# Kernel tuning notes

Hardware: AMD Instinct MI355X
Metric: run time of the kernel (lower is better)

The kernel has to match this reference:

```python
import jax, jax.numpy as jnp
import numpy as np

E = 262144   # num edges
T = 1048576  # num triplets
H = 128      # hidden_channels
IE = 64      # int_emb_size
NR = 6       # num_radial
NS = 7       # num_spherical
BD = 8       # basis_emb_size_dist
BA = 8       # basis_emb_size_angle


def setup_inputs() -> dict:
    key = jax.random.key(0)
    ks = jax.random.split(key, 32)
    def rnd(k, shape, s=0.1):
        return jax.random.normal(k, shape, dtype=jnp.float32) * s
    return {
        "x1": rnd(ks[0], (T, H), 1.0),
        "x_old": rnd(ks[1], (E, H), 1.0),
        "rbf0": rnd(ks[2], (E, NR), 1.0),
        "sbf": rnd(ks[3], (T, NS * NR), 1.0),
        "idx_kj": jax.random.randint(ks[4], (T,), 0, E),
        "idx_ji": jax.random.randint(ks[5], (T,), 0, E),
        "W_rbf1": rnd(ks[6], (NR, BD)),
        "W_rbf2": rnd(ks[7], (BD, H)),
        "W_sbf1": rnd(ks[8], (NS * NR, BA)),
        "W_sbf2": rnd(ks[9], (BA, IE)),
        "W_rbf": rnd(ks[10], (NR, H)),
        "W_kj": rnd(ks[11], (H, H)), "b_kj": rnd(ks[12], (H,)),
        "W_ji": rnd(ks[13], (H, H)), "b_ji": rnd(ks[14], (H,)),
        "W_connect": rnd(ks[15], (H, H)), "b_connect": rnd(ks[16], (H,)),
        "W_get_up": rnd(ks[17], (H, H)), "b_get_up": rnd(ks[18], (H,)),
        "W_down": rnd(ks[19], (H, IE)), "b_down": rnd(ks[20], (IE,)),
        "W_up": rnd(ks[21], (IE, H)), "b_up": rnd(ks[22], (H,)),
        "res_before_W": rnd(ks[23], (1, 2, H, H)), "res_before_b": rnd(ks[24], (1, 2, H)),
        "W_lin": rnd(ks[25], (H, H)), "b_lin": rnd(ks[26], (H,)),
        "res_after_W": rnd(ks[27], (2, 2, H, H)), "res_after_b": rnd(ks[28], (2, 2, H)),
    }


def _residual(x, W, b):
    # x + act(lin2(act(lin1(x))))
    h = jax.nn.silu(x @ W[0] + b[0])
    return x + jax.nn.silu(h @ W[1] + b[1])


def reference(x1, x_old, rbf0, sbf, idx_kj, idx_ji, W_rbf1, W_rbf2, W_sbf1, W_sbf2,
              W_rbf, W_kj, b_kj, W_ji, b_ji, W_connect, b_connect, W_get_up, b_get_up,
              W_down, b_down, W_up, b_up, res_before_W, res_before_b, W_lin, b_lin,
              res_after_W, res_after_b):
    act = jax.nn.silu  # swish
    nE = x_old.shape[0]
    # aggregate plane features onto edges
    x_up = jax.ops.segment_sum(x1, idx_ji, num_segments=nE)
    x_up = act(x_up @ W_get_up + b_get_up)
    x_ji = act(x_old @ W_ji + b_ji)
    x_kj = act(x_old @ W_kj + b_kj)
    rbf = (rbf0 @ W_rbf1) @ W_rbf2            # [E, H]
    x_kj = x_kj * rbf
    x_kj = act(x_kj @ W_down + b_down)        # [E, IE]
    sbf_p = (sbf @ W_sbf1) @ W_sbf2           # [T, IE]
    x_kj = x_kj[idx_kj] * sbf_p               # gather edges -> triplets
    x_kj = jax.ops.segment_sum(x_kj, idx_ji, num_segments=nE)  # scatter back to edges
    x_kj = act(x_kj @ W_up + b_up)
    e1 = x_ji + x_kj
    e1 = act(e1 @ W_connect + b_connect) + x_up
    for i in range(res_before_W.shape[0]):
        e1 = _residual(e1, res_before_W[i], res_before_b[i])
    e1 = act(e1 @ W_lin + b_lin) + x_old
    for i in range(res_after_W.shape[0]):
        e1 = _residual(e1, res_after_W[i], res_after_b[i])
    e2 = (rbf0 @ W_rbf) * e1
    return (e1, e2)
```

## Files before the change

### kernel.cpp

```cpp
#include <hip/hip_runtime.h>

#define E_N 262144
#define T_N 1048576

typedef short  bf16x8  __attribute__((ext_vector_type(8)));
typedef float  f32x4   __attribute__((ext_vector_type(4)));

#define OFF_KJ    0
#define OFF_DOWN  16384
#define OFF_UP    24576
#define OFF_JI    32768
#define OFF_GU    49152
#define OFF_CN    65536
#define OFF_RB0   81920
#define OFF_RB1   98304
#define OFF_LIN   114688
#define OFF_RA00  131072
#define OFF_RA01  147456
#define OFF_RA10  163840
#define OFF_RA11  180224
#define OFF_END   196608
#define WREG_BYTES 524288u

#define OFFB_AGG   0u
#define OFFB_XKJ   33554432u
#define OFFB_WREG  67108864u
#define OFFB_CNT   67633152u
#define OFFB_POS   68683776u
#define OFFB_TRI   69732352u
#define OFFB_BS    73926656u
#define OFFB_BP    73927680u
#define OFFB_KJP   75497472u
#define OFFB_INV   79691776u

__device__ __forceinline__ float silu_f(float x) {
  float e;
  asm("v_exp_f32_e32 %0, %1" : "=v"(e) : "v"(x * -1.44269504088896f));
  float r;
  asm("v_rcp_f32_e32 %0, %1" : "=v"(r) : "v"(1.0f + e));
  return x * r;
}

__device__ __forceinline__ unsigned short f2bf(float f) {
  union { float f; unsigned int u; } v; v.f = f;
  unsigned int u = v.u;
  return (unsigned short)((u + 0x7fffu + ((u >> 16) & 1u)) >> 16);
}
__device__ __forceinline__ float bf2f(unsigned short h) {
  union { unsigned int u; float f; } v; v.u = ((unsigned int)h) << 16;
  return v.f;
}

__device__ __forceinline__ unsigned cvtpk(float lo, float hi) {
  unsigned r;
  asm("v_cvt_pk_bf16_f32 %0, %1, %2" : "=v"(r) : "v"(lo), "v"(hi));
  return r;
}

template<int NC, int NR, int NTH>
__device__ __forceinline__ void stage_tile(const float* __restrict__ g, char* __restrict__ lds) {
  constexpr int RB = NC * 2;
  constexpr int C4 = NC / 4;
  for (int i = threadIdx.x; i < NR * C4; i += NTH) {
    int r = i / C4, c4 = i % C4;
    float4 v = *(const float4*)(g + (size_t)r * NC + c4 * 4);
    uint2 u;
    u.x = cvtpk(v.x, v.y);
    u.y = cvtpk(v.z, v.w);
    *(uint2*)(lds + r * RB + ((c4 * 8) ^ ((r & 7) << 4))) = u;
  }
}

template<int MREP, int NREP, int KSTEPS, int RB>
__device__ __forceinline__ void mfma_gemm(const char* __restrict__ lds, int row0, int col0,
                                          const unsigned short* __restrict__ WT, int lane,
                                          f32x4 (&acc)[MREP][NREP]) {
  const int kg = lane >> 4, r15 = lane & 15;
#pragma unroll
  for (int m = 0; m < MREP; ++m)
#pragma unroll
    for (int n = 0; n < NREP; ++n) acc[m][n] = (f32x4){0.f, 0.f, 0.f, 0.f};
  __builtin_amdgcn_s_setprio(1);
#pragma unroll
  for (int kk = 0; kk < KSTEPS; ++kk) {
    bf16x8 a[MREP], bfr[NREP];
#pragma unroll
    for (int m = 0; m < MREP; ++m) {
      int row = row0 + m * 16 + r15;
      a[m] = *(const bf16x8*)(lds + row * RB + ((kk * 64 + kg * 16) ^ ((row & 7) << 4)));
    }
#pragma unroll
    for (int n = 0; n < NREP; ++n) {
      int nc = col0 + n * 16 + r15;
      bfr[n] = *(const bf16x8*)((const short*)WT + nc * (KSTEPS * 32) + kk * 32 + kg * 8);
    }
#pragma unroll
    for (int m = 0; m < MREP; ++m)
#pragma unroll
      for (int n = 0; n < NREP; ++n)
        acc[m][n] = __builtin_amdgcn_mfma_f32_16x16x32_bf16(a[m], bfr[n], acc[m][n], 0, 0, 0);
  }
  __builtin_amdgcn_s_setprio(0);
}

template<int MREP, int NREP, int KSTEPS, int RS>
__device__ __forceinline__ void mfma_gemm_gA(const unsigned short* __restrict__ gA,
                                             int row0, int col0,
                                             const unsigned short* __restrict__ WT, int lane,
                                             f32x4 (&acc)[MREP][NREP]) {
  const int kg = lane >> 4, r15 = lane & 15;
#pragma unroll
  for (int m = 0; m < MREP; ++m)
#pragma unroll
    for (int n = 0; n < NREP; ++n) acc[m][n] = (f32x4){0.f, 0.f, 0.f, 0.f};
  __builtin_amdgcn_s_setprio(1);
#pragma unroll
  for (int kk = 0; kk < KSTEPS; ++kk) {
    bf16x8 a[MREP], bfr[NREP];
#pragma unroll
    for (int m = 0; m < MREP; ++m)
      a[m] = *(const bf16x8*)(gA + (size_t)(row0 + m * 16 + r15) * RS + kk * 32 + kg * 8);
#pragma unroll
    for (int n = 0; n < NREP; ++n) {
      int nc = col0 + n * 16 + r15;
      bfr[n] = *(const bf16x8*)((const short*)WT + nc * (KSTEPS * 32) + kk * 32 + kg * 8);
    }
#pragma unroll
    for (int m = 0; m < MREP; ++m)
#pragma unroll
      for (int n = 0; n < NREP; ++n)
        acc[m][n] = __builtin_amdgcn_mfma_f32_16x16x32_bf16(a[m], bfr[n], acc[m][n], 0, 0, 0);
  }
  __builtin_amdgcn_s_setprio(0);
}

template<int RB>
__device__ __forceinline__ void write_cd(char* __restrict__ lds, int wrow, int wcol, int lane,
                                         const f32x4 (&v)[2][2]) {
  const int kg = lane >> 4, r15 = lane & 15;
#pragma unroll
  for (int m = 0; m < 2; ++m)
#pragma unroll
    for (int n = 0; n < 2; ++n) {
      int col2 = (wcol + n * 16 + r15) * 2;
      int row0 = wrow + m * 16 + kg * 4;
      unsigned u0 = cvtpk(v[m][n][0], v[m][n][1]);
      unsigned u1 = cvtpk(v[m][n][2], v[m][n][3]);
      *(unsigned short*)(lds + (row0 + 0) * RB + (col2 ^ (((row0 + 0) & 7) << 4))) = (unsigned short)u0;
      *(unsigned short*)(lds + (row0 + 1) * RB + (col2 ^ (((row0 + 1) & 7) << 4))) = (unsigned short)(u0 >> 16);
      *(unsigned short*)(lds + (row0 + 2) * RB + (col2 ^ (((row0 + 2) & 7) << 4))) = (unsigned short)u1;
      *(unsigned short*)(lds + (row0 + 3) * RB + (col2 ^ (((row0 + 3) & 7) << 4))) = (unsigned short)(u1 >> 16);
    }
}

__global__ void __launch_bounds__(256) k_prep(
    const float* __restrict__ W_kj, const float* __restrict__ W_down,
    const float* __restrict__ W_up, const float* __restrict__ W_ji,
    const float* __restrict__ W_get_up, const float* __restrict__ W_connect,
    const float* __restrict__ rbW, const float* __restrict__ W_lin,
    const float* __restrict__ raW,
    const float* __restrict__ W_rbf1, const float* __restrict__ W_rbf2,
    unsigned short* __restrict__ wreg) {
  int b = blockIdx.x;
  if (b == 13) {
    float* W12 = (float*)(wreg + OFF_END);
    for (int i = threadIdx.x; i < 768; i += 256) {
      int r = i >> 7, n = i & 127;
      float s = 0.f;
#pragma unroll
      for (int q = 0; q < 8; ++q) s += W_rbf1[r * 8 + q] * W_rbf2[q * 128 + n];
      W12[i] = s;
    }
    return;
  }
  const float* src; int K = 128, N = 128; int off;
  switch (b) {
    case 0:  src = W_kj;          off = OFF_KJ;  break;
    case 1:  src = W_down;        off = OFF_DOWN; N = 64;  break;
    case 2:  src = W_up;          off = OFF_UP;   K = 64;  break;
    case 3:  src = W_ji;          off = OFF_JI;  break;
    case 4:  src = W_get_up;      off = OFF_GU;  break;
    case 5:  src = W_connect;     off = OFF_CN;  break;
    case 6:  src = rbW;           off = OFF_RB0; break;
    case 7:  src = rbW + 16384;   off = OFF_RB1; break;
    case 8:  src = W_lin;         off = OFF_LIN; break;
    case 9:  src = raW;           off = OFF_RA00; break;
    case 10: src = raW + 16384;   off = OFF_RA01; break;
    case 11: src = raW + 32768;   off = OFF_RA10; break;
    default: src = raW + 49152;   off = OFF_RA11; break;
  }
  unsigned short* dst = wreg + off;
  for (int i = threadIdx.x; i < K * N; i += 256) {
    int k = i / N, n = i % N;
    dst[n * K + k] = f2bf(src[i]);
  }
}

__global__ void __launch_bounds__(256) k_hist(const int* __restrict__ idx_ji,
                                              int* __restrict__ counts) {
  int t = blockIdx.x * 256 + threadIdx.x;
  atomicAdd(&counts[idx_ji[t]], 1);
}

__global__ void __launch_bounds__(1024) k_scan1(const int* __restrict__ counts,
                                                int* __restrict__ locpre,
                                                int* __restrict__ bsum) {
  __shared__ int s[1024];
  int i = blockIdx.x * 1024 + threadIdx.x;
  int v = counts[i];
  s[threadIdx.x] = v; __syncthreads();
  for (int o = 1; o < 1024; o <<= 1) {
    int t = (threadIdx.x >= o) ? s[threadIdx.x - o] : 0;
    __syncthreads();
    s[threadIdx.x] += t;
    __syncthreads();
  }
  locpre[i] = s[threadIdx.x] - v;
  if (threadIdx.x == 1023) bsum[blockIdx.x] = s[1023];
}

__global__ void __launch_bounds__(256) k_scan2(const int* __restrict__ bsum,
                                               int* __restrict__ bpre, int* __restrict__ offs) {
  __shared__ int s[256];
  int v = bsum[threadIdx.x];
  s[threadIdx.x] = v; __syncthreads();
  for (int o = 1; o < 256; o <<= 1) {
    int t = (threadIdx.x >= o) ? s[threadIdx.x - o] : 0;
    __syncthreads();
    s[threadIdx.x] += t;
    __syncthreads();
  }
  bpre[threadIdx.x] = s[threadIdx.x] - v;
  if (threadIdx.x == 0) offs[E_N] = T_N;
}

__global__ void __launch_bounds__(1024) k_scan3(const int* __restrict__ locpre,
                                                const int* __restrict__ bpre,
                                                int* __restrict__ offs,
                                                int* __restrict__ pos) {
  int i = blockIdx.x * 1024 + threadIdx.x;
  int v = locpre[i] + bpre[blockIdx.x];
  offs[i] = v;
  pos[i] = v;
}

__global__ void __launch_bounds__(256) k_fill(const int* __restrict__ idx_ji,
                                              const int* __restrict__ idx_kj,
                                              int* __restrict__ pos,
                                              int* __restrict__ tri,
                                              int* __restrict__ inv,
                                              int* __restrict__ kjp) {
  int t = blockIdx.x * 256 + threadIdx.x;
  int e = idx_ji[t];
  int slot = atomicAdd(&pos[e], 1);
  tri[slot] = t;
  inv[t] = slot;
  kjp[slot] = idx_kj[t];
}

__global__ void __launch_bounds__(256) k_sbfp(const float* __restrict__ sbf,
                                              const float* __restrict__ W_sbf1,
                                              const float* __restrict__ W_sbf2,
                                              const int* __restrict__ inv,
                                              unsigned int* __restrict__ sbfp) {
  __shared__ float s_s[336];
  __shared__ float s_t8[8][8];
  int t0 = blockIdx.x * 8;
  const float4* src = (const float4*)(sbf + (size_t)t0 * 42);
  for (int i = threadIdx.x; i < 84; i += 256)
    ((float4*)s_s)[i] = src[i];
  __syncthreads();
  if (threadIdx.x < 64) {
    int w8 = threadIdx.x >> 3, bb = threadIdx.x & 7;
    float s = 0.f;
#pragma unroll
    for (int r = 0; r < 42; ++r) s += s_s[w8 * 42 + r] * W_sbf1[r * 8 + bb];
    s_t8[w8][bb] = s;
  }
  __syncthreads();
  int w8 = threadIdx.x >> 5, jj = threadIdx.x & 31;
  float sp0 = 0.f, sp1 = 0.f;
#pragma unroll
  for (int bb = 0; bb < 8; ++bb) {
    float tv = s_t8[w8][bb];
    sp0 += tv * W_sbf2[bb * 64 + jj * 2];
    sp1 += tv * W_sbf2[bb * 64 + jj * 2 + 1];
  }
  int slot = inv[t0 + w8];
  sbfp[(size_t)slot * 32 + jj] = cvtpk(sp0, sp1);
}

__global__ void __launch_bounds__(256) k_aggB(const int* __restrict__ offs,
                                              const int* __restrict__ kjp,
                                              const unsigned int* __restrict__ sbfp,
                                              const unsigned int* __restrict__ xkj,
                                              unsigned int* __restrict__ agg) {
  int sub = threadIdx.x >> 5, jj = threadIdx.x & 31;
  int e = blockIdx.x * 8 + sub;
  int o0 = offs[e], o1 = offs[e + 1];
  float a0 = 0.f, a1 = 0.f;
  for (int i = o0; i < o1; ++i) {
    int kj = kjp[i];
    unsigned int sv = sbfp[(size_t)i * 32 + jj];
    unsigned int xv = xkj[(size_t)kj * 32 + jj];
    a0 += bf2f((unsigned short)(sv & 0xffff)) * bf2f((unsigned short)(xv & 0xffff));
    a1 += bf2f((unsigned short)(sv >> 16)) * bf2f((unsigned short)(xv >> 16));
  }
  agg[(size_t)e * 32 + jj] = cvtpk(a0, a1);
}

__global__ void __launch_bounds__(256) k_xupg(const int* __restrict__ offs,
                                              const int* __restrict__ tri,
                                              const float* __restrict__ x1,
                                              unsigned int* __restrict__ out) {
  int sub = threadIdx.x >> 6, h2 = threadIdx.x & 63;
  int e = blockIdx.x * 4 + sub;
  int o0 = offs[e], o1 = offs[e + 1];
  float a0 = 0.f, a1 = 0.f;
  for (int i = o0; i < o1; ++i) {
    int t = tri[i];
    float2 v = *(const float2*)(x1 + (size_t)t * 128 + h2 * 2);
    a0 += v.x; a1 += v.y;
  }
  out[(size_t)e * 128 + h2] = cvtpk(a0, a1);
}

__global__ void __launch_bounds__(512, 4) phaseA(
    const float* __restrict__ x_old, const float* __restrict__ rbf0,
    const unsigned short* __restrict__ wreg,
    const float* __restrict__ b_kj, const float* __restrict__ b_down,
    unsigned short* __restrict__ xkjdown) {
  __shared__ char lds[32768];
  char* B0 = lds;
  char* B1 = lds + 16384;
  const int tid = threadIdx.x, lane = tid & 63, wave = tid >> 6;
  const int kg = lane >> 4, r15 = lane & 15;
  const int wrow = (wave >> 2) * 32, wcol = (wave & 3) * 32;
  const size_t e_base = (size_t)blockIdx.x * 64;
  const float* W12 = (const float*)(wreg + OFF_END);

  stage_tile<128, 64, 512>(x_old + e_base * 128, B0);
  __syncthreads();

  f32x4 acc[2][2], val[2][2];
  mfma_gemm<2, 2, 4, 256>(B0, wrow, wcol, wreg + OFF_KJ, lane, acc);
#pragma unroll
  for (int n = 0; n < 2; ++n) {
    int col = wcol + n * 16 + r15;
    float bk = b_kj[col];
    float wc[6];
#pragma unroll
    for (int q = 0; q < 6; ++q) wc[q] = W12[q * 128 + col];
#pragma unroll
    for (int m = 0; m < 2; ++m)
#pragma unroll
      for (int r = 0; r < 4; ++r) {
        int row = wrow + m * 16 + kg * 4 + r;
        const float* rp = rbf0 + (e_base + row) * 6;
        float rv = rp[0]*wc[0] + rp[1]*wc[1] + rp[2]*wc[2] + rp[3]*wc[3] + rp[4]*wc[4] + rp[5]*wc[5];
        val[m][n][r] = silu_f(acc[m][n][r] + bk) * rv;
      }
  }
  write_cd<256>(B1, wrow, wcol, lane, val);
  __syncthreads();

  const int wrow2 = (wave >> 1) * 16, wcol2 = (wave & 1) * 32;
  f32x4 a2[1][2];
  mfma_gemm<1, 2, 4, 256>(B1, wrow2, wcol2, wreg + OFF_DOWN, lane, a2);
#pragma unroll
  for (int n = 0; n < 2; ++n) {
    int col = wcol2 + n * 16 + r15;
    float bd = b_down[col];
#pragma unroll
    for (int r = 0; r < 4; ++r) {
      int row = wrow2 + kg * 4 + r;
      xkjdown[(e_base + row) * 64 + col] = f2bf(silu_f(a2[0][n][r] + bd));
    }
  }
}

__global__ void __launch_bounds__(512, 4) phaseC1(
    const float* __restrict__ x_old, float* __restrict__ e1buf,
    const unsigned short* __restrict__ xup_b,
    const unsigned short* __restrict__ agg, const unsigned short* __restrict__ wreg,
    const float* __restrict__ b_up, const float* __restrict__ b_ji,
    const float* __restrict__ b_get_up, const float* __restrict__ b_connect,
    const float* __restrict__ rbB, const float* __restrict__ b_lin,
    const float* __restrict__ raB,
    const float* __restrict__ rbf0, const float* __restrict__ W_rbf,
    float* __restrict__ e2o) {
  __shared__ char lds[32768];
  char* X0 = lds;
  char* X1 = lds + 16384;
  const int tid = threadIdx.x, lane = tid & 63, wave = tid >> 6;
  const int kg = lane >> 4, r15 = lane & 15;
  const int wrow = (wave >> 2) * 32, wcol = (wave & 3) * 32;
  const size_t e_base = (size_t)blockIdx.x * 64;

  stage_tile<128, 64, 512>(x_old + e_base * 128, X1);
  __syncthreads();

  f32x4 acc[2][2], keep[2][2], h[2][2];

  mfma_gemm_gA<2, 2, 2, 64>(agg + e_base * 64, wrow, wcol, wreg + OFF_UP, lane, acc);
#pragma unroll
  for (int n = 0; n < 2; ++n) {
    float bu = b_up[wcol + n * 16 + r15];
#pragma unroll
    for (int m = 0; m < 2; ++m)
#pragma unroll
      for (int r = 0; r < 4; ++r) h[m][n][r] = silu_f(acc[m][n][r] + bu);
  }
  mfma_gemm<2, 2, 4, 256>(X1, wrow, wcol, wreg + OFF_JI, lane, acc);
#pragma unroll
  for (int n = 0; n < 2; ++n) {
    float bj = b_ji[wcol + n * 16 + r15];
#pragma unroll
    for (int m = 0; m < 2; ++m)
#pragma unroll
      for (int r = 0; r < 4; ++r) keep[m][n][r] = silu_f(acc[m][n][r] + bj) + h[m][n][r];
  }
  write_cd<256>(X0, wrow, wcol, lane, keep);
  __syncthreads();

  mfma_gemm_gA<2, 2, 4, 256>(xup_b + e_base * 256, wrow, wcol, wreg + OFF_GU, lane, acc);
#pragma unroll
  for (int n = 0; n < 2; ++n) {
    float bg = b_get_up[wcol + n * 16 + r15];
#pragma unroll
    for (int m = 0; m < 2; ++m)
#pragma unroll
      for (int r = 0; r < 4; ++r) h[m][n][r] = silu_f(acc[m][n][r] + bg);
  }
  mfma_gemm<2, 2, 4, 256>(X0, wrow, wcol, wreg + OFF_CN, lane, acc);
#pragma unroll
  for (int n = 0; n < 2; ++n) {
    float bc = b_connect[wcol + n * 16 + r15];
#pragma unroll
    for (int m = 0; m < 2; ++m)
#pragma unroll
      for (int r = 0; r < 4; ++r) keep[m][n][r] = silu_f(acc[m][n][r] + bc) + h[m][n][r];
  }
  write_cd<256>(X1, wrow, wcol, lane, keep);
  __syncthreads();

  mfma_gemm<2, 2, 4, 256>(X1, wrow, wcol, wreg + OFF_RB0, lane, acc);
#pragma unroll
  for (int n = 0; n < 2; ++n) {
    float bv = rbB[wcol + n * 16 + r15];
#pragma unroll
    for (int m = 0; m < 2; ++m)
#pragma unroll
      for (int r = 0; r < 4; ++r) h[m][n][r] = silu_f(acc[m][n][r] + bv);
  }
  write_cd<256>(X0, wrow, wcol, lane, h);
  __syncthreads();

  mfma_gemm<2, 2, 4, 256>(X0, wrow, wcol, wreg + OFF_RB1, lane, acc);
#pragma unroll
  for (int n = 0; n < 2; ++n) {
    float bv = rbB[128 + wcol + n * 16 + r15];
#pragma unroll
    for (int m = 0; m < 2; ++m)
#pragma unroll
      for (int r = 0; r < 4; ++r) keep[m][n][r] += silu_f(acc[m][n][r] + bv);
  }
  write_cd<256>(X1, wrow, wcol, lane, keep);
  __syncthreads();

  mfma_gemm<2, 2, 4, 256>(X1, wrow, wcol, wreg + OFF_LIN, lane, acc);
#pragma unroll
  for (int n = 0; n < 2; ++n) {
    int col = wcol + n * 16 + r15;
    float bl = b_lin[col];
#pragma unroll
    for (int m = 0; m < 2; ++m)
#pragma unroll
      for (int r = 0; r < 4; ++r) {
        int row = wrow + m * 16 + kg * 4 + r;
        keep[m][n][r] = silu_f(acc[m][n][r] + bl) + x_old[(e_base + row) * 128 + col];
      }
  }
  write_cd<256>(X0, wrow, wcol, lane, keep);
  __syncthreads();

  mfma_gemm<2, 2, 4, 256>(X0, wrow, wcol, wreg + OFF_RA00, lane, acc);
#pragma unroll
  for (int n = 0; n < 2; ++n) {
    float bv = raB[wcol + n * 16 + r15];
#pragma unroll
    for (int m = 0; m < 2; ++m)
#pragma unroll
      for (int r = 0; r < 4; ++r) h[m][n][r] = silu_f(acc[m][n][r] + bv);
  }
  write_cd<256>(X1, wrow, wcol, lane, h);
  __syncthreads();

  mfma_gemm<2, 2, 4, 256>(X1, wrow, wcol, wreg + OFF_RA01, lane, acc);
#pragma unroll
  for (int n = 0; n < 2; ++n) {
    float bv = raB[128 + wcol + n * 16 + r15];
#pragma unroll
    for (int m = 0; m < 2; ++m)
#pragma unroll
      for (int r = 0; r < 4; ++r) keep[m][n][r] += silu_f(acc[m][n][r] + bv);
  }
  write_cd<256>(X0, wrow, wcol, lane, keep);
  __syncthreads();

  mfma_gemm<2, 2, 4, 256>(X0, wrow, wcol, wreg + OFF_RA10, lane, acc);
#pragma unroll
  for (int n = 0; n < 2; ++n) {
    float bv = raB[256 + wcol + n * 16 + r15];
#pragma unroll
    for (int m = 0; m < 2; ++m)
#pragma unroll
      for (int r = 0; r < 4; ++r) h[m][n][r] = silu_f(acc[m][n][r] + bv);
  }
  write_cd<256>(X1, wrow, wcol, lane, h);
  __syncthreads();

  mfma_gemm<2, 2, 4, 256>(X1, wrow, wcol, wreg + OFF_RA11, lane, acc);
#pragma unroll
  for (int n = 0; n < 2; ++n) {
    int col = wcol + n * 16 + r15;
    float bv = raB[384 + col];
    float wc[6];
#pragma unroll
    for (int q = 0; q < 6; ++q) wc[q] = W_rbf[q * 128 + col];
#pragma unroll
    for (int m = 0; m < 2; ++m)
#pragma unroll
      for (int r = 0; r < 4; ++r) {
        int row = wrow + m * 16 + kg * 4 + r;
        size_t e = e_base + row;
        float val = keep[m][n][r] + silu_f(acc[m][n][r] + bv);
        e1buf[e * 128 + col] = val;
        if (e2o) {
          const float* rp = rbf0 + e * 6;
          float rv = rp[0]*wc[0] + rp[1]*wc[1] + rp[2]*wc[2] + rp[3]*wc[3] + rp[4]*wc[4] + rp[5]*wc[5];
          e2o[e * 128 + col] = val * rv;
        }
      }
  }
}

__global__ void __launch_bounds__(256) k_e2(const float* __restrict__ e1,
                                            const float* __restrict__ rbf0,
                                            const float* __restrict__ W_rbf,
                                            float* __restrict__ e2) {
  size_t gid = (size_t)blockIdx.x * 256 + threadIdx.x;
  int e = (int)(gid >> 5);
  int c = (int)(gid & 31) << 2;
  float r6[6];
#pragma unroll
  for (int r = 0; r < 6; ++r) r6[r] = rbf0[(size_t)e * 6 + r];
  float4 v = *(const float4*)(e1 + (size_t)e * 128 + c);
  float4 o;
  float rv;
  rv = 0.f;
#pragma unroll
  for (int r = 0; r < 6; ++r) rv += r6[r] * W_rbf[r * 128 + c + 0];
  o.x = v.x * rv;
  rv = 0.f;
#pragma unroll
  for (int r = 0; r < 6; ++r) rv += r6[r] * W_rbf[r * 128 + c + 1];
  o.y = v.y * rv;
  rv = 0.f;
#pragma unroll
  for (int r = 0; r < 6; ++r) rv += r6[r] * W_rbf[r * 128 + c + 2];
  o.z = v.z * rv;
  rv = 0.f;
#pragma unroll
  for (int r = 0; r < 6; ++r) rv += r6[r] * W_rbf[r * 128 + c + 3];
  o.w = v.w * rv;
  *(float4*)(e2 + (size_t)e * 128 + c) = o;
}

extern "C" void kernel_launch(void* const* d_in, const int* in_sizes, int n_in,
                              void* d_out, int out_size, void* d_ws, size_t ws_size,
                              hipStream_t stream) {
  const float* x1        = (const float*)d_in[0];
  const float* x_old     = (const float*)d_in[1];
  const float* rbf0      = (const float*)d_in[2];
  const float* sbf       = (const float*)d_in[3];
  const int*   idx_kj    = (const int*)d_in[4];
  const int*   idx_ji    = (const int*)d_in[5];
  const float* W_rbf1    = (const float*)d_in[6];
  const float* W_rbf2    = (const float*)d_in[7];
  const float* W_sbf1    = (const float*)d_in[8];
  const float* W_sbf2    = (const float*)d_in[9];
  const float* W_rbf     = (const float*)d_in[10];
  const float* W_kj      = (const float*)d_in[11];
  const float* b_kj      = (const float*)d_in[12];
  const float* W_ji      = (const float*)d_in[13];
  const float* b_ji      = (const float*)d_in[14];
  const float* W_connect = (const float*)d_in[15];
  const float* b_connect = (const float*)d_in[16];
  const float* W_get_up  = (const float*)d_in[17];
  const float* b_get_up  = (const float*)d_in[18];
  const float* W_down    = (const float*)d_in[19];
  const float* b_down    = (const float*)d_in[20];
  const float* W_up      = (const float*)d_in[21];
  const float* b_up      = (const float*)d_in[22];
  const float* rbW       = (const float*)d_in[23];
  const float* rbB       = (const float*)d_in[24];
  const float* W_lin     = (const float*)d_in[25];
  const float* b_lin     = (const float*)d_in[26];
  const float* raW       = (const float*)d_in[27];
  const float* raB       = (const float*)d_in[28];

  float* e1buf = (float*)d_out;
  char*  base2 = (char*)d_out + (size_t)E_N * 128 * 4;
  float* e2out = (float*)base2;

  unsigned short* xkj_b = (unsigned short*)(base2 + OFFB_XKJ);
  int* counts = (int*)(base2 + OFFB_CNT);
  int* pos    = (int*)(base2 + OFFB_POS);
  int* tri    = (int*)(base2 + OFFB_TRI);
  int* bsum   = (int*)(base2 + OFFB_BS);
  int* bpre   = (int*)(base2 + OFFB_BP);
  int* kjp    = (int*)(base2 + OFFB_KJP);
  int* inv    = (int*)(base2 + OFFB_INV);

  const size_t need_ws = (size_t)WREG_BYTES + (size_t)E_N * 64 * 2;
  const bool fuse = ws_size >= need_ws;
  unsigned short* wreg  = fuse ? (unsigned short*)d_ws
                               : (unsigned short*)(base2 + OFFB_WREG);
  unsigned short* agg_b = fuse ? (unsigned short*)((char*)d_ws + WREG_BYTES)
                               : (unsigned short*)(base2 + OFFB_AGG);

  unsigned int* sbfp_u = (unsigned int*)e1buf;
  unsigned int* xup_u  = (unsigned int*)e1buf;

  k_prep<<<14, 256, 0, stream>>>(W_kj, W_down, W_up, W_ji, W_get_up, W_connect,
                                 rbW, W_lin, raW, W_rbf1, W_rbf2, wreg);

  hipMemsetAsync(counts, 0, (E_N + 1) * sizeof(int), stream);
  k_hist<<<T_N / 256, 256, 0, stream>>>(idx_ji, counts);
  k_scan1<<<256, 1024, 0, stream>>>(counts, pos, bsum);
  k_scan2<<<1, 256, 0, stream>>>(bsum, bpre, counts);
  k_scan3<<<256, 1024, 0, stream>>>(pos, bpre, counts, pos);
  k_fill<<<T_N / 256, 256, 0, stream>>>(idx_ji, idx_kj, pos, tri, inv, kjp);

  k_sbfp<<<T_N / 8, 256, 0, stream>>>(sbf, W_sbf1, W_sbf2, inv, sbfp_u);

  phaseA<<<E_N / 64, 512, 0, stream>>>(x_old, rbf0, wreg, b_kj, b_down, xkj_b);

  k_aggB<<<E_N / 8, 256, 0, stream>>>(counts, kjp, sbfp_u,
                                      (const unsigned int*)xkj_b, (unsigned int*)agg_b);

  k_xupg<<<E_N / 4, 256, 0, stream>>>(counts, tri, x1, xup_u);

  phaseC1<<<E_N / 64, 512, 0, stream>>>(x_old, e1buf, (const unsigned short*)xup_u,
                                        agg_b, wreg,
                                        b_up, b_ji, b_get_up, b_connect, rbB, b_lin, raB,
                                        rbf0, W_rbf, fuse ? e2out : nullptr);
  if (!fuse)
    k_e2<<<E_N * 32 / 256, 256, 0, stream>>>(e1buf, rbf0, W_rbf, e2out);
}
```

Before: 1.279 ms.

## Retile phaseC1 to 128-edge blocks of 1024 threads with 64x16 wave tiles

The fused edge MLP chain kernel now handles 128 edges per block with 16 waves instead of 64 edges with 8 waves. Each wave computes a 64x16 output tile (four M repeats, one N repeat) instead of 32x32, and the LDS ping-pong buffers double to 64KB. The goal is fewer blocks and more B-fragment reuse across M per weight load, at the cost of larger LDS per block, fewer resident blocks per CU, and more A-operand loads from LDS per wave.

```diff
diff --git a/kernel.cpp b/kernel.cpp
--- a/kernel.cpp
+++ b/kernel.cpp
@@ -134,14 +134,14 @@
   __builtin_amdgcn_s_setprio(0);
 }
 
-template<int RB>
+template<int MREP, int NREP, int RB>
 __device__ __forceinline__ void write_cd(char* __restrict__ lds, int wrow, int wcol, int lane,
-                                         const f32x4 (&v)[2][2]) {
+                                         const f32x4 (&v)[MREP][NREP]) {
   const int kg = lane >> 4, r15 = lane & 15;
 #pragma unroll
-  for (int m = 0; m < 2; ++m)
-#pragma unroll
-    for (int n = 0; n < 2; ++n) {
+  for (int m = 0; m < MREP; ++m)
+#pragma unroll
+    for (int n = 0; n < NREP; ++n) {
       int col2 = (wcol + n * 16 + r15) * 2;
       int row0 = wrow + m * 16 + kg * 4;
       unsigned u0 = cvtpk(v[m][n][0], v[m][n][1]);
@@ -361,7 +361,7 @@
         val[m][n][r] = silu_f(acc[m][n][r] + bk) * rv;
       }
   }
-  write_cd<256>(B1, wrow, wcol, lane, val);
+  write_cd<2, 2, 256>(B1, wrow, wcol, lane, val);
   __syncthreads();
 
   const int wrow2 = (wave >> 1) * 16, wcol2 = (wave & 1) * 32;
@@ -379,7 +379,7 @@
   }
 }
 
-__global__ void __launch_bounds__(512, 4) phaseC1(
+__global__ void __launch_bounds__(1024, 4) phaseC1(
     const float* __restrict__ x_old, float* __restrict__ e1buf,
     const unsigned short* __restrict__ xup_b,
     const unsigned short* __restrict__ agg, const unsigned short* __restrict__ wreg,
@@ -389,152 +389,141 @@
     const float* __restrict__ raB,
     const float* __restrict__ rbf0, const float* __restrict__ W_rbf,
     float* __restrict__ e2o) {
-  __shared__ char lds[32768];
+  __shared__ char lds[65536];
   char* X0 = lds;
-  char* X1 = lds + 16384;
+  char* X1 = lds + 32768;
   const int tid = threadIdx.x, lane = tid & 63, wave = tid >> 6;
   const int kg = lane >> 4, r15 = lane & 15;
-  const int wrow = (wave >> 2) * 32, wcol = (wave & 3) * 32;
-  const size_t e_base = (size_t)blockIdx.x * 64;
-
-  stage_tile<128, 64, 512>(x_old + e_base * 128, X1);
-  __syncthreads();
-
-  f32x4 acc[2][2], keep[2][2], h[2][2];
-
-  mfma_gemm_gA<2, 2, 2, 64>(agg + e_base * 64, wrow, wcol, wreg + OFF_UP, lane, acc);
-#pragma unroll
-  for (int n = 0; n < 2; ++n) {
-    float bu = b_up[wcol + n * 16 + r15];
-#pragma unroll
-    for (int m = 0; m < 2; ++m)
-#pragma unroll
-      for (int r = 0; r < 4; ++r) h[m][n][r] = silu_f(acc[m][n][r] + bu);
-  }
-  mfma_gemm<2, 2, 4, 256>(X1, wrow, wcol, wreg + OFF_JI, lane, acc);
-#pragma unroll
-  for (int n = 0; n < 2; ++n) {
-    float bj = b_ji[wcol + n * 16 + r15];
-#pragma unroll
-    for (int m = 0; m < 2; ++m)
-#pragma unroll
-      for (int r = 0; r < 4; ++r) keep[m][n][r] = silu_f(acc[m][n][r] + bj) + h[m][n][r];
-  }
-  write_cd<256>(X0, wrow, wcol, lane, keep);
-  __syncthreads();
-
-  mfma_gemm_gA<2, 2, 4, 256>(xup_b + e_base * 256, wrow, wcol, wreg + OFF_GU, lane, acc);
-#pragma unroll
-  for (int n = 0; n < 2; ++n) {
-    float bg = b_get_up[wcol + n * 16 + r15];
-#pragma unroll
-    for (int m = 0; m < 2; ++m)
-#pragma unroll
-      for (int r = 0; r < 4; ++r) h[m][n][r] = silu_f(acc[m][n][r] + bg);
-  }
-  mfma_gemm<2, 2, 4, 256>(X0, wrow, wcol, wreg + OFF_CN, lane, acc);
-#pragma unroll
-  for (int n = 0; n < 2; ++n) {
-    float bc = b_connect[wcol + n * 16 + r15];
-#pragma unroll
-    for (int m = 0; m < 2; ++m)
-#pragma unroll
-      for (int r = 0; r < 4; ++r) keep[m][n][r] = silu_f(acc[m][n][r] + bc) + h[m][n][r];
-  }
-  write_cd<256>(X1, wrow, wcol, lane, keep);
-  __syncthreads();
-
-  mfma_gemm<2, 2, 4, 256>(X1, wrow, wcol, wreg + OFF_RB0, lane, acc);
-#pragma unroll
-  for (int n = 0; n < 2; ++n) {
-    float bv = rbB[wcol + n * 16 + r15];
-#pragma unroll
-    for (int m = 0; m < 2; ++m)
-#pragma unroll
-      for (int r = 0; r < 4; ++r) h[m][n][r] = silu_f(acc[m][n][r] + bv);
-  }
-  write_cd<256>(X0, wrow, wcol, lane, h);
-  __syncthreads();
-
-  mfma_gemm<2, 2, 4, 256>(X0, wrow, wcol, wreg + OFF_RB1, lane, acc);
-#pragma unroll
-  for (int n = 0; n < 2; ++n) {
-    float bv = rbB[128 + wcol + n * 16 + r15];
-#pragma unroll
-    for (int m = 0; m < 2; ++m)
-#pragma unroll
-      for (int r = 0; r < 4; ++r) keep[m][n][r] += silu_f(acc[m][n][r] + bv);
-  }
-  write_cd<256>(X1, wrow, wcol, lane, keep);
-  __syncthreads();
-
-  mfma_gemm<2, 2, 4, 256>(X1, wrow, wcol, wreg + OFF_LIN, lane, acc);
-#pragma unroll
-  for (int n = 0; n < 2; ++n) {
-    int col = wcol + n * 16 + r15;
+  const int wrow = (wave >> 3) * 64;
+  const int wcol = (wave & 7) * 16;
+  const size_t e_base = (size_t)blockIdx.x * 128;
+
+  stage_tile<128, 128, 1024>(x_old + e_base * 128, X1);
+  __syncthreads();
+
+  f32x4 acc[4][1], keep[4][1], h[4][1];
+
+  mfma_gemm_gA<4, 1, 2, 64>(agg + e_base * 64, wrow, wcol, wreg + OFF_UP, lane, acc);
+#pragma unroll
+  for (int m = 0; m < 4; ++m) {
+    float bu = b_up[wcol + r15];
+#pragma unroll
+    for (int r = 0; r < 4; ++r) h[m][0][r] = silu_f(acc[m][0][r] + bu);
+  }
+  mfma_gemm<4, 1, 4, 256>(X1, wrow, wcol, wreg + OFF_JI, lane, acc);
+  {
+    float bj = b_ji[wcol + r15];
+#pragma unroll
+    for (int m = 0; m < 4; ++m)
+#pragma unroll
+      for (int r = 0; r < 4; ++r) keep[m][0][r] = silu_f(acc[m][0][r] + bj) + h[m][0][r];
+  }
+  write_cd<4, 1, 256>(X0, wrow, wcol, lane, keep);
+  __syncthreads();
+
+  mfma_gemm_gA<4, 1, 4, 256>(xup_b + e_base * 256, wrow, wcol, wreg + OFF_GU, lane, acc);
+  {
+    float bg = b_get_up[wcol + r15];
+#pragma unroll
+    for (int m = 0; m < 4; ++m)
+#pragma unroll
+      for (int r = 0; r < 4; ++r) h[m][0][r] = silu_f(acc[m][0][r] + bg);
+  }
+  mfma_gemm<4, 1, 4, 256>(X0, wrow, wcol, wreg + OFF_CN, lane, acc);
+  {
+    float bc = b_connect[wcol + r15];
+#pragma unroll
+    for (int m = 0; m < 4; ++m)
+#pragma unroll
+      for (int r = 0; r < 4; ++r) keep[m][0][r] = silu_f(acc[m][0][r] + bc) + h[m][0][r];
+  }
+  write_cd<4, 1, 256>(X1, wrow, wcol, lane, keep);
+  __syncthreads();
+
+  mfma_gemm<4, 1, 4, 256>(X1, wrow, wcol, wreg + OFF_RB0, lane, acc);
+  {
+    float bv = rbB[wcol + r15];
+#pragma unroll
+    for (int m = 0; m < 4; ++m)
+#pragma unroll
+      for (int r = 0; r < 4; ++r) h[m][0][r] = silu_f(acc[m][0][r] + bv);
+  }
+  write_cd<4, 1, 256>(X0, wrow, wcol, lane, h);
+  __syncthreads();
+
+  mfma_gemm<4, 1, 4, 256>(X0, wrow, wcol, wreg + OFF_RB1, lane, acc);
+  {
+    float bv = rbB[128 + wcol + r15];
+#pragma unroll
+    for (int m = 0; m < 4; ++m)
+#pragma unroll
+      for (int r = 0; r < 4; ++r) keep[m][0][r] += silu_f(acc[m][0][r] + bv);
+  }
+  write_cd<4, 1, 256>(X1, wrow, wcol, lane, keep);
+  __syncthreads();
+
+  mfma_gemm<4, 1, 4, 256>(X1, wrow, wcol, wreg + OFF_LIN, lane, acc);
+  {
+    int col = wcol + r15;
     float bl = b_lin[col];
 #pragma unroll
-    for (int m = 0; m < 2; ++m)
+    for (int m = 0; m < 4; ++m)
 #pragma unroll
       for (int r = 0; r < 4; ++r) {
         int row = wrow + m * 16 + kg * 4 + r;
-        keep[m][n][r] = silu_f(acc[m][n][r] + bl) + x_old[(e_base + row) * 128 + col];
+        keep[m][0][r] = silu_f(acc[m][0][r] + bl) + x_old[(e_base + row) * 128 + col];
       }
   }
-  write_cd<256>(X0, wrow, wcol, lane, keep);
-  __syncthreads();
-
-  mfma_gemm<2, 2, 4, 256>(X0, wrow, wcol, wreg + OFF_RA00, lane, acc);
-#pragma unroll
-  for (int n = 0; n < 2; ++n) {
-    float bv = raB[wcol + n * 16 + r15];
-#pragma unroll
-    for (int m = 0; m < 2; ++m)
-#pragma unroll
-      for (int r = 0; r < 4; ++r) h[m][n][r] = silu_f(acc[m][n][r] + bv);
-  }
-  write_cd<256>(X1, wrow, wcol, lane, h);
-  __syncthreads();
-
-  mfma_gemm<2, 2, 4, 256>(X1, wrow, wcol, wreg + OFF_RA01, lane, acc);
-#pragma unroll
-  for (int n = 0; n < 2; ++n) {
-    float bv = raB[128 + wcol + n * 16 + r15];
-#pragma unroll
-    for (int m = 0; m < 2; ++m)
-#pragma unroll
-      for (int r = 0; r < 4; ++r) keep[m][n][r] += silu_f(acc[m][n][r] + bv);
-  }
-  write_cd<256>(X0, wrow, wcol, lane, keep);
-  __syncthreads();
-
-  mfma_gemm<2, 2, 4, 256>(X0, wrow, wcol, wreg + OFF_RA10, lane, acc);
-#pragma unroll
-  for (int n = 0; n < 2; ++n) {
-    float bv = raB[256 + wcol + n * 16 + r15];
-#pragma unroll
-    for (int m = 0; m < 2; ++m)
-#pragma unroll
-      for (int r = 0; r < 4; ++r) h[m][n][r] = silu_f(acc[m][n][r] + bv);
-  }
-  write_cd<256>(X1, wrow, wcol, lane, h);
-  __syncthreads();
-
-  mfma_gemm<2, 2, 4, 256>(X1, wrow, wcol, wreg + OFF_RA11, lane, acc);
-#pragma unroll
-  for (int n = 0; n < 2; ++n) {
-    int col = wcol + n * 16 + r15;
+  write_cd<4, 1, 256>(X0, wrow, wcol, lane, keep);
+  __syncthreads();
+
+  mfma_gemm<4, 1, 4, 256>(X0, wrow, wcol, wreg + OFF_RA00, lane, acc);
+  {
+    float bv = raB[wcol + r15];
+#pragma unroll
+    for (int m = 0; m < 4; ++m)
+#pragma unroll
+      for (int r = 0; r < 4; ++r) h[m][0][r] = silu_f(acc[m][0][r] + bv);
+  }
+  write_cd<4, 1, 256>(X1, wrow, wcol, lane, h);
+  __syncthreads();
+
+  mfma_gemm<4, 1, 4, 256>(X1, wrow, wcol, wreg + OFF_RA01, lane, acc);
+  {
+    float bv = raB[128 + wcol + r15];
+#pragma unroll
+    for (int m = 0; m < 4; ++m)
+#pragma unroll
+      for (int r = 0; r < 4; ++r) keep[m][0][r] += silu_f(acc[m][0][r] + bv);
+  }
+  write_cd<4, 1, 256>(X0, wrow, wcol, lane, keep);
+  __syncthreads();
+
+  mfma_gemm<4, 1, 4, 256>(X0, wrow, wcol, wreg + OFF_RA10, lane, acc);
+  {
+    float bv = raB[256 + wcol + r15];
+#pragma unroll
+    for (int m = 0; m < 4; ++m)
+#pragma unroll
+      for (int r = 0; r < 4; ++r) h[m][0][r] = silu_f(acc[m][0][r] + bv);
+  }
+  write_cd<4, 1, 256>(X1, wrow, wcol, lane, h);
+  __syncthreads();
+
+  mfma_gemm<4, 1, 4, 256>(X1, wrow, wcol, wreg + OFF_RA11, lane, acc);
+  {
+    int col = wcol + r15;
     float bv = raB[384 + col];
     float wc[6];
 #pragma unroll
     for (int q = 0; q < 6; ++q) wc[q] = W_rbf[q * 128 + col];
 #pragma unroll
-    for (int m = 0; m < 2; ++m)
+    for (int m = 0; m < 4; ++m)
 #pragma unroll
       for (int r = 0; r < 4; ++r) {
         int row = wrow + m * 16 + kg * 4 + r;
         size_t e = e_base + row;
-        float val = keep[m][n][r] + silu_f(acc[m][n][r] + bv);
+        float val = keep[m][0][r] + silu_f(acc[m][0][r] + bv);
         e1buf[e * 128 + col] = val;
         if (e2o) {
           const float* rp = rbf0 + e * 6;
@@ -652,10 +641,10 @@
 
   k_xupg<<<E_N / 4, 256, 0, stream>>>(counts, tri, x1, xup_u);
 
-  phaseC1<<<E_N / 64, 512, 0, stream>>>(x_old, e1buf, (const unsigned short*)xup_u,
-                                        agg_b, wreg,
-                                        b_up, b_ji, b_get_up, b_connect, rbB, b_lin, raB,
-                                        rbf0, W_rbf, fuse ? e2out : nullptr);
+  phaseC1<<<E_N / 128, 1024, 0, stream>>>(x_old, e1buf, (const unsigned short*)xup_u,
+                                          agg_b, wreg,
+                                          b_up, b_ji, b_get_up, b_connect, rbB, b_lin, raB,
+                                          rbf0, W_rbf, fuse ? e2out : nullptr);
   if (!fuse)
     k_e2<<<E_N * 32 / 256, 256, 0, stream>>>(e1buf, rbf0, W_rbf, e2out);
 }
```

After: 1.234 ms. -3.5%, faster.
